# Performance work log

Measured on AMD Instinct MI355X. Metric: run time of the kernel, lower is better.

## Reference

```python
import jax, jax.numpy as jnp
import numpy as np

B, S, HID, H = 8, 1024, 1024, 16
D = HID // H  # dim per head = 64

def setup_inputs() -> dict:
    key = jax.random.key(0)
    ks = jax.random.split(key, 7)
    s = 1.0 / np.sqrt(D)  # mimic nn.Linear uniform init scale
    return {
        "sequences": jax.random.normal(ks[0], (B, S, HID), dtype=jnp.float32),
        "Wq": jax.random.uniform(ks[1], (H, D, D), jnp.float32, -s, s),
        "bq": jax.random.uniform(ks[2], (H, D), jnp.float32, -s, s),
        "Wk": jax.random.uniform(ks[3], (H, D, D), jnp.float32, -s, s),
        "bk": jax.random.uniform(ks[4], (H, D), jnp.float32, -s, s),
        "Wv": jax.random.uniform(ks[5], (H, D, D), jnp.float32, -s, s),
        "bv": jax.random.uniform(ks[6], (H, D), jnp.float32, -s, s),
    }

def reference(sequences, Wq, bq, Wk, bk, Wv, bv):
    # per-head input slice h is sequences[:, :, h*D:(h+1)*D] == reshape
    x = sequences.reshape(B, S, H, D)
    # torch Linear: y = x @ W.T + b, W is [out, in] -> einsum 'bshd,hed->bshe'
    q = jnp.einsum('bshd,hed->bshe', x, Wq) + bq
    k = jnp.einsum('bshd,hed->bshe', x, Wk) + bk
    v = jnp.einsum('bshd,hed->bshe', x, Wv) + bv
    scores = jnp.einsum('bshe,bthe->bhst', q, k) / jnp.sqrt(jnp.float32(D))
    attn = jax.nn.softmax(scores, axis=-1)  # [B,H,S,S]
    out = jnp.einsum('bhst,bthe->bshe', attn, v)
    return out.reshape(B, S, HID)  # hstack of heads == reshape
```

## Files before the change

### kernel.cpp

```cpp
#include <hip/hip_runtime.h>
#include <hip/hip_bf16.h>

#define B_   8
#define S_   1024
#define HID_ 1024
#define H_   16
#define D_   64

typedef __hip_bfloat16 bf16;
typedef __attribute__((ext_vector_type(8))) short s16x8;
typedef __attribute__((ext_vector_type(4))) float f32x4;

#define QK_BH 65536
#define V_BH  65536

__device__ __forceinline__ short f2b(float f) {
    union { float f; unsigned u; } a; a.f = f;
    return (short)((a.u + 0x8000u) >> 16);
}
__device__ __forceinline__ s16x8 cvt8(const float* p) {
    const float4* q = (const float4*)p;
    float4 u = q[0], v = q[1];
    s16x8 r;
    r[0] = f2b(u.x); r[1] = f2b(u.y); r[2] = f2b(u.z); r[3] = f2b(u.w);
    r[4] = f2b(v.x); r[5] = f2b(v.y); r[6] = f2b(v.z); r[7] = f2b(v.w);
    return r;
}
__device__ __forceinline__ s16x8 load8bf(const bf16* p) {
    return *(const s16x8*)p;
}

__global__ __launch_bounds__(256) void cvt_w(
    const float* __restrict__ Wq, const float* __restrict__ Wk,
    const float* __restrict__ Wv, bf16* __restrict__ Wf)
{
    const float* srcs[3] = {Wq, Wk, Wv};
    const float* src = srcs[blockIdx.y];
    bf16* dst = Wf + (size_t)blockIdx.y * (H_ * D_ * D_);
    const int i = blockIdx.x * 256 + threadIdx.x;
    const int h = i >> 9;
    const int r = i & 511;
    const int et = r >> 7, half = (r >> 6) & 1, lane = r & 63;
    const int quad = lane >> 4, c = lane & 15;
    const float* s = src + h * 4096 + (et * 16 + c) * 64 + half * 32 + quad * 8;
    bf16* d = dst + h * 4096 + et * 1024 + half * 512 + lane * 8;
    *(s16x8*)d = cvt8(s);
}

__global__ __launch_bounds__(256) void qkv_proj(
    const float* __restrict__ x, const bf16* __restrict__ Wf,
    const float* __restrict__ bq, const float* __restrict__ bk,
    const float* __restrict__ bv,
    bf16* __restrict__ Qf, bf16* __restrict__ Kf, bf16* __restrict__ Vf)
{
    __shared__ __align__(16) bf16 xs[128][72];

    const int id = blockIdx.x;
    const int bh_i = id & 127, sc = id >> 7;
    const int b = bh_i >> 4, h = bh_i & 15;
    const int t = threadIdx.x;
    const int wave = t >> 6, lane = t & 63;
    const int quad = lane >> 4, c = lane & 15;
    const size_t bh = (size_t)bh_i;

    {
        const float* xg = x + ((size_t)b * S_ + sc * 128) * HID_ + h * D_;
#pragma unroll
        for (int i = 0; i < 8; ++i) {
            const int j = i * 256 + t;
            const int row = j >> 4, seg = j & 15;
            float4 v = *(const float4*)(xg + (size_t)row * HID_ + seg * 4);
            short4 pk;
            pk.x = f2b(v.x); pk.y = f2b(v.y); pk.z = f2b(v.z); pk.w = f2b(v.w);
            *(short4*)&xs[row][seg * 4] = pk;
        }
    }
    __syncthreads();

    s16x8 xa[2][2];
#pragma unroll
    for (int mt = 0; mt < 2; ++mt) {
        xa[mt][0] = *(const s16x8*)&xs[wave * 32 + mt * 16 + c][quad * 8];
        xa[mt][1] = *(const s16x8*)&xs[wave * 32 + mt * 16 + c][32 + quad * 8];
    }

    const float* bs[3] = {bq, bk, bv};

#pragma unroll
    for (int m = 0; m < 3; ++m) {
        const bf16*  Wm   = Wf + ((size_t)m * H_ + h) * 4096;
        const float* bias = bs[m] + h * D_;
#pragma unroll
        for (int et = 0; et < 4; ++et) {
            s16x8 wf0 = load8bf(Wm + et * 1024 + lane * 8);
            s16x8 wf1 = load8bf(Wm + et * 1024 + 512 + lane * 8);
            if (m < 2) {
                const int hp = et >> 1;
                const int qp = (2 * et + (quad >> 1)) & 3;
                const float4 bb = *(const float4*)&bias[et * 16 + quad * 4];
                bf16* base = (m == 0 ? Qf : Kf) + bh * QK_BH;
#pragma unroll
                for (int mt = 0; mt < 2; ++mt) {
                    f32x4 acc = {0.f, 0.f, 0.f, 0.f};
                    acc = __builtin_amdgcn_mfma_f32_16x16x32_bf16(wf0, xa[mt][0], acc, 0, 0, 0);
                    acc = __builtin_amdgcn_mfma_f32_16x16x32_bf16(wf1, xa[mt][1], acc, 0, 0, 0);
                    const int ts = sc * 8 + wave * 2 + mt;
                    bf16* dst = base + ts * 1024 + hp * 512 +
                                (qp * 16 + c) * 8 + (quad & 1) * 4;
                    short4 pk;
                    pk.x = f2b(acc[0] + bb.x);
                    pk.y = f2b(acc[1] + bb.y);
                    pk.z = f2b(acc[2] + bb.z);
                    pk.w = f2b(acc[3] + bb.w);
                    *(short4*)dst = pk;
                }
            } else {
                const float bbv = bias[et * 16 + c];
                const int kt = sc * 2 + (wave >> 1);
                const int p  = wave & 1;
                bf16* base = Vf + bh * V_BH + kt * 4096 + et * 1024 + p * 512;
#pragma unroll
                for (int mt = 0; mt < 2; ++mt) {
                    f32x4 acc = {0.f, 0.f, 0.f, 0.f};
                    acc = __builtin_amdgcn_mfma_f32_16x16x32_bf16(xa[mt][0], wf0, acc, 0, 0, 0);
                    acc = __builtin_amdgcn_mfma_f32_16x16x32_bf16(xa[mt][1], wf1, acc, 0, 0, 0);
                    bf16* dst = base + (quad * 16 + c) * 8 + mt * 4;
                    short4 pk;
                    pk.x = f2b(acc[0] + bbv);
                    pk.y = f2b(acc[1] + bbv);
                    pk.z = f2b(acc[2] + bbv);
                    pk.w = f2b(acc[3] + bbv);
                    *(short4*)dst = pk;
                }
            }
        }
    }
}

__global__ __launch_bounds__(256, 3) void attn(
    const bf16* __restrict__ Qf, const bf16* __restrict__ Kf,
    const bf16* __restrict__ Vf, float* __restrict__ out)
{
    __shared__ __align__(16) float os[4][16][68];

    const int id = blockIdx.x;
    const int bh_i = id & 127, qc = id >> 7;
    const int b = bh_i >> 4, h = bh_i & 15;
    const int wave = threadIdx.x >> 6, lane = threadIdx.x & 63;
    const int quad = lane >> 4, c = lane & 15;
    const int q0 = qc * 128 + wave * 32;
    const size_t bh = (size_t)bh_i;

    s16x8 aq[2][2];
#pragma unroll
    for (int mt = 0; mt < 2; ++mt) {
        const bf16* Qb = Qf + bh * QK_BH + (qc * 8 + wave * 2 + mt) * 1024 + lane * 8;
        aq[mt][0] = load8bf(Qb);
        aq[mt][1] = load8bf(Qb + 512);
    }

    f32x4 o[2][4], ol[2];
#pragma unroll
    for (int mt = 0; mt < 2; ++mt) {
#pragma unroll
        for (int et = 0; et < 4; ++et) o[mt][et] = {0.f, 0.f, 0.f, 0.f};
        ol[mt] = {0.f, 0.f, 0.f, 0.f};
    }

    s16x8 ones;
#pragma unroll
    for (int j = 0; j < 8; ++j) ones[j] = (short)0x3F80;

    const float CEXP = 0.18033688011112042f;
    const float NM0  = -16.0f * 0.18033688011112042f;

    const bf16* Kb = Kf + bh * QK_BH + lane * 8;
    const bf16* Vb = Vf + bh * V_BH  + lane * 8;

#pragma unroll 1
    for (int kt = 0; kt < S_ / 64; ++kt) {
        s16x8 ka[4], kb2[4];
#pragma unroll
        for (int ct = 0; ct < 4; ++ct) {
            ka[ct]  = load8bf(Kb + (kt * 4 + ct) * 1024);
            kb2[ct] = load8bf(Kb + (kt * 4 + ct) * 1024 + 512);
        }
        s16x8 vf4[4][2];
#pragma unroll
        for (int et = 0; et < 4; ++et)
#pragma unroll
            for (int p = 0; p < 2; ++p)
                vf4[et][p] = load8bf(Vb + kt * 4096 + et * 1024 + p * 512);

        f32x4 s[2][4];
#pragma unroll
        for (int mt = 0; mt < 2; ++mt)
#pragma unroll
            for (int ct = 0; ct < 4; ++ct) {
                f32x4 acc = {0.f, 0.f, 0.f, 0.f};
                acc = __builtin_amdgcn_mfma_f32_16x16x32_bf16(ka[ct],  aq[mt][0], acc, 0, 0, 0);
                acc = __builtin_amdgcn_mfma_f32_16x16x32_bf16(kb2[ct], aq[mt][1], acc, 0, 0, 0);
                s[mt][ct] = acc;
            }

        s16x8 pz[2][2];
#pragma unroll
        for (int mt = 0; mt < 2; ++mt) {
#pragma unroll
            for (int p = 0; p < 2; ++p) {
                s16x8 z;
#pragma unroll
                for (int j = 0; j < 4; ++j) {
                    float pa = __builtin_amdgcn_exp2f(fmaf(s[mt][2 * p][j],     CEXP, NM0));
                    float pb = __builtin_amdgcn_exp2f(fmaf(s[mt][2 * p + 1][j], CEXP, NM0));
                    z[j]     = f2b(pa);
                    z[4 + j] = f2b(pb);
                }
                pz[mt][p] = z;
                ol[mt] = __builtin_amdgcn_mfma_f32_16x16x32_bf16(z, ones, ol[mt], 0, 0, 0);
            }
        }

#pragma unroll
        for (int mt = 0; mt < 2; ++mt)
#pragma unroll
            for (int et = 0; et < 4; ++et) {
                o[mt][et] = __builtin_amdgcn_mfma_f32_16x16x32_bf16(pz[mt][0], vf4[et][0], o[mt][et], 0, 0, 0);
                o[mt][et] = __builtin_amdgcn_mfma_f32_16x16x32_bf16(pz[mt][1], vf4[et][1], o[mt][et], 0, 0, 0);
            }
    }

#pragma unroll
    for (int mt = 0; mt < 2; ++mt) {
        float inv[4];
#pragma unroll
        for (int r = 0; r < 4; ++r) inv[r] = 1.0f / ol[mt][r];
#pragma unroll
        for (int et = 0; et < 4; ++et)
#pragma unroll
            for (int r = 0; r < 4; ++r)
                os[wave][quad * 4 + r][et * 16 + c] = o[mt][et][r] * inv[r];
        float* orow = out + ((size_t)b * S_ + q0 + mt * 16 + c) * HID_ + h * D_;
#pragma unroll
        for (int j = 0; j < 4; ++j) {
            float4 v = *(const float4*)&os[wave][c][(quad + j * 4) * 4];
            *(float4*)(orow + (quad + j * 4) * 4) = v;
        }
    }
}

extern "C" void kernel_launch(void* const* d_in, const int* in_sizes, int n_in,
                              void* d_out, int out_size, void* d_ws, size_t ws_size,
                              hipStream_t stream) {
    (void)in_sizes; (void)n_in; (void)out_size; (void)ws_size;
    const float* x  = (const float*)d_in[0];
    const float* Wq = (const float*)d_in[1];
    const float* bq = (const float*)d_in[2];
    const float* Wk = (const float*)d_in[3];
    const float* bk = (const float*)d_in[4];
    const float* Wv = (const float*)d_in[5];
    const float* bv = (const float*)d_in[6];
    float* outp = (float*)d_out;

    bf16* Qfw = (bf16*)d_ws;
    bf16* Kfw = Qfw + (size_t)128 * QK_BH;
    bf16* Vfw = Kfw + (size_t)128 * QK_BH;
    bf16* Wfw = Vfw + (size_t)128 * V_BH;

    cvt_w<<<dim3(32, 3), 256, 0, stream>>>(Wq, Wk, Wv, Wfw);
    qkv_proj<<<dim3(1024), 256, 0, stream>>>(x, Wfw, bq, bk, bv, Qfw, Kfw, Vfw);
    attn<<<dim3(1024), 256, 0, stream>>>(Qfw, Kfw, Vfw, outp);
}
```

Before: 163.7 us.

## Enlarge attention query tile, compute row sums in VALU, halve projection tile

The attention kernel now gives each wave four 16-row query tiles instead of two. Each K/V tile loaded per iteration is reused across twice as many queries, and the grid shrinks to 512 blocks with occupancy lowered to 2. The softmax denominator moves from an MFMA against a ones vector to scalar adds plus cross-lane shuffles at the end, which frees matrix-core cycles. The projection kernel is split into 64-row chunks over 2048 blocks for more parallelism. Higher register pressure and fewer attention blocks on the GPU could hurt latency hiding.

```diff
diff --git a/kernel.cpp b/kernel.cpp
--- a/kernel.cpp
+++ b/kernel.cpp
@@ -53,7 +53,7 @@
     const float* __restrict__ bv,
     bf16* __restrict__ Qf, bf16* __restrict__ Kf, bf16* __restrict__ Vf)
 {
-    __shared__ __align__(16) bf16 xs[128][72];
+    __shared__ __align__(16) bf16 xs[64][72];
 
     const int id = blockIdx.x;
     const int bh_i = id & 127, sc = id >> 7;
@@ -64,9 +64,9 @@
     const size_t bh = (size_t)bh_i;
 
     {
-        const float* xg = x + ((size_t)b * S_ + sc * 128) * HID_ + h * D_;
-#pragma unroll
-        for (int i = 0; i < 8; ++i) {
+        const float* xg = x + ((size_t)b * S_ + sc * 64) * HID_ + h * D_;
+#pragma unroll
+        for (int i = 0; i < 4; ++i) {
             const int j = i * 256 + t;
             const int row = j >> 4, seg = j & 15;
             float4 v = *(const float4*)(xg + (size_t)row * HID_ + seg * 4);
@@ -77,12 +77,8 @@
     }
     __syncthreads();
 
-    s16x8 xa[2][2];
-#pragma unroll
-    for (int mt = 0; mt < 2; ++mt) {
-        xa[mt][0] = *(const s16x8*)&xs[wave * 32 + mt * 16 + c][quad * 8];
-        xa[mt][1] = *(const s16x8*)&xs[wave * 32 + mt * 16 + c][32 + quad * 8];
-    }
+    s16x8 xa0 = *(const s16x8*)&xs[wave * 16 + c][quad * 8];
+    s16x8 xa1 = *(const s16x8*)&xs[wave * 16 + c][32 + quad * 8];
 
     const float* bs[3] = {bq, bk, bv};
 
@@ -98,46 +94,37 @@
                 const int hp = et >> 1;
                 const int qp = (2 * et + (quad >> 1)) & 3;
                 const float4 bb = *(const float4*)&bias[et * 16 + quad * 4];
-                bf16* base = (m == 0 ? Qf : Kf) + bh * QK_BH;
-#pragma unroll
-                for (int mt = 0; mt < 2; ++mt) {
-                    f32x4 acc = {0.f, 0.f, 0.f, 0.f};
-                    acc = __builtin_amdgcn_mfma_f32_16x16x32_bf16(wf0, xa[mt][0], acc, 0, 0, 0);
-                    acc = __builtin_amdgcn_mfma_f32_16x16x32_bf16(wf1, xa[mt][1], acc, 0, 0, 0);
-                    const int ts = sc * 8 + wave * 2 + mt;
-                    bf16* dst = base + ts * 1024 + hp * 512 +
-                                (qp * 16 + c) * 8 + (quad & 1) * 4;
-                    short4 pk;
-                    pk.x = f2b(acc[0] + bb.x);
-                    pk.y = f2b(acc[1] + bb.y);
-                    pk.z = f2b(acc[2] + bb.z);
-                    pk.w = f2b(acc[3] + bb.w);
-                    *(short4*)dst = pk;
-                }
+                f32x4 acc = {0.f, 0.f, 0.f, 0.f};
+                acc = __builtin_amdgcn_mfma_f32_16x16x32_bf16(wf0, xa0, acc, 0, 0, 0);
+                acc = __builtin_amdgcn_mfma_f32_16x16x32_bf16(wf1, xa1, acc, 0, 0, 0);
+                const int ts = sc * 4 + wave;
+                bf16* dst = (m == 0 ? Qf : Kf) + bh * QK_BH + ts * 1024 +
+                            hp * 512 + (qp * 16 + c) * 8 + (quad & 1) * 4;
+                short4 pk;
+                pk.x = f2b(acc[0] + bb.x);
+                pk.y = f2b(acc[1] + bb.y);
+                pk.z = f2b(acc[2] + bb.z);
+                pk.w = f2b(acc[3] + bb.w);
+                *(short4*)dst = pk;
             } else {
                 const float bbv = bias[et * 16 + c];
-                const int kt = sc * 2 + (wave >> 1);
-                const int p  = wave & 1;
-                bf16* base = Vf + bh * V_BH + kt * 4096 + et * 1024 + p * 512;
-#pragma unroll
-                for (int mt = 0; mt < 2; ++mt) {
-                    f32x4 acc = {0.f, 0.f, 0.f, 0.f};
-                    acc = __builtin_amdgcn_mfma_f32_16x16x32_bf16(xa[mt][0], wf0, acc, 0, 0, 0);
-                    acc = __builtin_amdgcn_mfma_f32_16x16x32_bf16(xa[mt][1], wf1, acc, 0, 0, 0);
-                    bf16* dst = base + (quad * 16 + c) * 8 + mt * 4;
-                    short4 pk;
-                    pk.x = f2b(acc[0] + bbv);
-                    pk.y = f2b(acc[1] + bbv);
-                    pk.z = f2b(acc[2] + bbv);
-                    pk.w = f2b(acc[3] + bbv);
-                    *(short4*)dst = pk;
-                }
-            }
-        }
-    }
-}
-
-__global__ __launch_bounds__(256, 3) void attn(
+                f32x4 acc = {0.f, 0.f, 0.f, 0.f};
+                acc = __builtin_amdgcn_mfma_f32_16x16x32_bf16(xa0, wf0, acc, 0, 0, 0);
+                acc = __builtin_amdgcn_mfma_f32_16x16x32_bf16(xa1, wf1, acc, 0, 0, 0);
+                bf16* dst = Vf + bh * V_BH + sc * 4096 + et * 1024 +
+                            (wave >> 1) * 512 + (quad * 16 + c) * 8 + (wave & 1) * 4;
+                short4 pk;
+                pk.x = f2b(acc[0] + bbv);
+                pk.y = f2b(acc[1] + bbv);
+                pk.z = f2b(acc[2] + bbv);
+                pk.w = f2b(acc[3] + bbv);
+                *(short4*)dst = pk;
+            }
+        }
+    }
+}
+
+__global__ __launch_bounds__(256, 2) void attn(
     const bf16* __restrict__ Qf, const bf16* __restrict__ Kf,
     const bf16* __restrict__ Vf, float* __restrict__ out)
 {
@@ -148,28 +135,23 @@
     const int b = bh_i >> 4, h = bh_i & 15;
     const int wave = threadIdx.x >> 6, lane = threadIdx.x & 63;
     const int quad = lane >> 4, c = lane & 15;
-    const int q0 = qc * 128 + wave * 32;
+    const int ts0 = qc * 16 + wave * 4;
     const size_t bh = (size_t)bh_i;
 
-    s16x8 aq[2][2];
-#pragma unroll
-    for (int mt = 0; mt < 2; ++mt) {
-        const bf16* Qb = Qf + bh * QK_BH + (qc * 8 + wave * 2 + mt) * 1024 + lane * 8;
+    s16x8 aq[4][2];
+#pragma unroll
+    for (int mt = 0; mt < 4; ++mt) {
+        const bf16* Qb = Qf + bh * QK_BH + (ts0 + mt) * 1024 + lane * 8;
         aq[mt][0] = load8bf(Qb);
         aq[mt][1] = load8bf(Qb + 512);
     }
 
-    f32x4 o[2][4], ol[2];
-#pragma unroll
-    for (int mt = 0; mt < 2; ++mt) {
+    f32x4 o[4][4];
+#pragma unroll
+    for (int mt = 0; mt < 4; ++mt)
 #pragma unroll
         for (int et = 0; et < 4; ++et) o[mt][et] = {0.f, 0.f, 0.f, 0.f};
-        ol[mt] = {0.f, 0.f, 0.f, 0.f};
-    }
-
-    s16x8 ones;
-#pragma unroll
-    for (int j = 0; j < 8; ++j) ones[j] = (short)0x3F80;
+    float l[4] = {0.f, 0.f, 0.f, 0.f};
 
     const float CEXP = 0.18033688011112042f;
     const float NM0  = -16.0f * 0.18033688011112042f;
@@ -192,55 +174,54 @@
             for (int p = 0; p < 2; ++p)
                 vf4[et][p] = load8bf(Vb + kt * 4096 + et * 1024 + p * 512);
 
-        f32x4 s[2][4];
-#pragma unroll
-        for (int mt = 0; mt < 2; ++mt)
+#pragma unroll
+        for (int mt = 0; mt < 4; ++mt) {
+            f32x4 s[4];
 #pragma unroll
             for (int ct = 0; ct < 4; ++ct) {
                 f32x4 acc = {0.f, 0.f, 0.f, 0.f};
                 acc = __builtin_amdgcn_mfma_f32_16x16x32_bf16(ka[ct],  aq[mt][0], acc, 0, 0, 0);
                 acc = __builtin_amdgcn_mfma_f32_16x16x32_bf16(kb2[ct], aq[mt][1], acc, 0, 0, 0);
-                s[mt][ct] = acc;
-            }
-
-        s16x8 pz[2][2];
-#pragma unroll
-        for (int mt = 0; mt < 2; ++mt) {
+                s[ct] = acc;
+            }
+            s16x8 pz[2];
 #pragma unroll
             for (int p = 0; p < 2; ++p) {
                 s16x8 z;
 #pragma unroll
                 for (int j = 0; j < 4; ++j) {
-                    float pa = __builtin_amdgcn_exp2f(fmaf(s[mt][2 * p][j],     CEXP, NM0));
-                    float pb = __builtin_amdgcn_exp2f(fmaf(s[mt][2 * p + 1][j], CEXP, NM0));
+                    float pa = __builtin_amdgcn_exp2f(fmaf(s[2 * p][j],     CEXP, NM0));
+                    float pb = __builtin_amdgcn_exp2f(fmaf(s[2 * p + 1][j], CEXP, NM0));
+                    l[mt] += pa + pb;
                     z[j]     = f2b(pa);
                     z[4 + j] = f2b(pb);
                 }
-                pz[mt][p] = z;
-                ol[mt] = __builtin_amdgcn_mfma_f32_16x16x32_bf16(z, ones, ol[mt], 0, 0, 0);
-            }
-        }
-
-#pragma unroll
-        for (int mt = 0; mt < 2; ++mt)
+                pz[p] = z;
+            }
 #pragma unroll
             for (int et = 0; et < 4; ++et) {
-                o[mt][et] = __builtin_amdgcn_mfma_f32_16x16x32_bf16(pz[mt][0], vf4[et][0], o[mt][et], 0, 0, 0);
-                o[mt][et] = __builtin_amdgcn_mfma_f32_16x16x32_bf16(pz[mt][1], vf4[et][1], o[mt][et], 0, 0, 0);
-            }
-    }
-
-#pragma unroll
-    for (int mt = 0; mt < 2; ++mt) {
+                o[mt][et] = __builtin_amdgcn_mfma_f32_16x16x32_bf16(pz[0], vf4[et][0], o[mt][et], 0, 0, 0);
+                o[mt][et] = __builtin_amdgcn_mfma_f32_16x16x32_bf16(pz[1], vf4[et][1], o[mt][et], 0, 0, 0);
+            }
+        }
+    }
+
+#pragma unroll
+    for (int mt = 0; mt < 4; ++mt) {
+        float L = l[mt];
+        L += __shfl_xor(L, 16, 64);
+        L += __shfl_xor(L, 32, 64);
+        const float Linv = 1.0f / L;
         float inv[4];
 #pragma unroll
-        for (int r = 0; r < 4; ++r) inv[r] = 1.0f / ol[mt][r];
+        for (int r = 0; r < 4; ++r)
+            inv[r] = __shfl(Linv, quad * 4 + r, 64);
 #pragma unroll
         for (int et = 0; et < 4; ++et)
 #pragma unroll
             for (int r = 0; r < 4; ++r)
                 os[wave][quad * 4 + r][et * 16 + c] = o[mt][et][r] * inv[r];
-        float* orow = out + ((size_t)b * S_ + q0 + mt * 16 + c) * HID_ + h * D_;
+        float* orow = out + ((size_t)b * S_ + (ts0 + mt) * 16 + c) * HID_ + h * D_;
 #pragma unroll
         for (int j = 0; j < 4; ++j) {
             float4 v = *(const float4*)&os[wave][c][(quad + j * 4) * 4];
@@ -268,6 +249,6 @@
     bf16* Wfw = Vfw + (size_t)128 * V_BH;
 
     cvt_w<<<dim3(32, 3), 256, 0, stream>>>(Wq, Wk, Wv, Wfw);
-    qkv_proj<<<dim3(1024), 256, 0, stream>>>(x, Wfw, bq, bk, bv, Qfw, Kfw, Vfw);
-    attn<<<dim3(1024), 256, 0, stream>>>(Qfw, Kfw, Vfw, outp);
-}
+    qkv_proj<<<dim3(2048), 256, 0, stream>>>(x, Wfw, bq, bk, bv, Qfw, Kfw, Vfw);
+    attn<<<dim3(512), 256, 0, stream>>>(Qfw, Kfw, Vfw, outp);
+}
```

Measured after the change: 145.4 us. 11.1% less time.
